# Kernel tuning notes

Hardware: AMD Instinct MI355X
Metric: run time of the kernel (lower is better)

Reference implementation:

```python
import jax, jax.numpy as jnp
import numpy as np

HEADS = 8

def _conv(x, w, b, stride, pad):
    # x: [B,C,H,W], w: [O,I,kh,kw] (torch OIHW layout)
    y = jax.lax.conv_general_dilated(x, w, (stride, stride), ((pad, pad), (pad, pad)),
                                     dimension_numbers=('NCHW', 'OIHW', 'NCHW'))
    return y + b[None, :, None, None]

def _maxpool2x2(x):
    # returns pooled values and one-hot argmax per 2x2 window (torch first-max tie-break)
    b, c, H, W = x.shape
    win = x.reshape(b, c, H // 2, 2, W // 2, 2).transpose(0, 1, 2, 4, 3, 5).reshape(b, c, H // 2, W // 2, 4)
    am = jnp.argmax(win, axis=-1)
    oh = jax.nn.one_hot(am, 4, dtype=x.dtype)
    pooled = jnp.sum(win * oh, axis=-1)
    return pooled, oh

def _maxunpool2x2(y, oh):
    b, c, h2, w2 = y.shape
    out = y[..., None] * oh  # [b,c,h2,w2,4]
    out = out.reshape(b, c, h2, w2, 2, 2).transpose(0, 1, 2, 4, 3, 5).reshape(b, c, h2 * 2, w2 * 2)
    return out

def _mha2d(x, wq, wk, wv, wo):
    # x: [b,c,h,w]; wq/wk/wv/wo stored as [in,out] so y = x @ W
    b, c, h, w = x.shape
    hw = h * w
    dk = wq.shape[1]
    dh = dk // HEADS
    xt = x.reshape(b, c, hw).transpose(0, 2, 1)  # [b,hw,c]
    def split(y):  # torch: view(b,hw,dh,heads).permute(0,3,1,2)
        return y.reshape(b, hw, dh, HEADS).transpose(0, 3, 1, 2)  # [b,heads,hw,dh]
    q = split(xt @ wq)
    k = split(xt @ wk)
    v = split(xt @ wv)
    scale = jnp.sqrt(jnp.asarray(dh, x.dtype))
    attn = jax.nn.softmax(jnp.einsum('bhqd,bhkd->bhqk', q, k) / scale, axis=-1)
    o = jnp.einsum('bhqk,bhkd->bhqd', attn, v)
    o = o.transpose(0, 2, 3, 1).reshape(b, hw, dk)  # [b,hw,dh,heads] -> merge
    o = o @ wo
    return o.transpose(0, 2, 1).reshape(b, dk, h, w)

def setup_inputs() -> dict:
    key = jax.random.key(0)
    ks = jax.random.split(key, 10)
    B, C, H, W = 16, 256, 64, 64
    s = 0.05
    return {
        'x': jax.random.normal(ks[0], (B, C, H, W), jnp.float32),
        'conv_w': jax.random.normal(ks[1], (C, C, 3, 3), jnp.float32) * s,
        'conv_b': jax.random.normal(ks[2], (C,), jnp.float32) * s,
        'fr_w': jax.random.normal(ks[3], (C, C, 1, 1), jnp.float32) * s,
        'fr_b': jax.random.normal(ks[4], (C,), jnp.float32) * s,
        'wq': jax.random.normal(ks[5], (C, C), jnp.float32) * s,
        'wk': jax.random.normal(ks[6], (C, C), jnp.float32) * s,
        'wv': jax.random.normal(ks[7], (C, C), jnp.float32) * s,
        'wo': jax.random.normal(ks[8], (C, C), jnp.float32) * s,
        'gamma': jax.random.normal(ks[9], (1,), jnp.float32) * 0.1,
    }

def reference(x, conv_w, conv_b, fr_w, fr_b, wq, wk, wv, wo, gamma):
    _x = _conv(x, fr_w, fr_b, 1, 0)          # 1x1 feature reduction
    _x, oh = _maxpool2x2(_x)                 # MaxPool2d(2, return_indices=True)
    _x = _mha2d(_x, wq, wk, wv, wo)          # attention over pooled grid
    _x = _maxunpool2x2(_x, oh)               # MaxUnpool2d(2)
    return _x * jnp.tanh(gamma[0]) + _conv(x, conv_w, conv_b, 1, 1)
```

## Files before the change

kernel.cpp:

```cpp
#include <hip/hip_runtime.h>
#include <hip/hip_bf16.h>
#include <math.h>

#define B 16
#define C 256
#define H 64
#define W 64
#define H2 32
#define W2 32
#define HW2 1024
#define HEADS 8
#define DH 32

typedef unsigned short ushort_t;
using short8 = __attribute__((ext_vector_type(8))) short;
using u16x8  = __attribute__((ext_vector_type(8))) unsigned short;
using f32x4  = __attribute__((ext_vector_type(4))) float;

__device__ inline ushort_t f2bf(float f) {
    __hip_bfloat16 hb = __float2bfloat16(f);
    return *(ushort_t*)&hb;
}
__device__ inline float bf2f(ushort_t u) {
    return __uint_as_float(((unsigned)u) << 16);
}

__device__ __forceinline__ void cp16(const ushort_t* g, ushort_t* l) {
    __builtin_amdgcn_global_load_lds(
        (const __attribute__((address_space(1))) void*)g,
        (__attribute__((address_space(3))) void*)l, 16, 0, 0);
}

#define RSCALE 0.17677669529663687f

__global__ __launch_bounds__(256) void k_prep_wT(const float* __restrict__ cw,
                                                 ushort_t* __restrict__ wbfT) {
    int i = threadIdx.x, o = blockIdx.x;
    const float* src = cw + ((size_t)o * C + i) * 9;
#pragma unroll
    for (int kk = 0; kk < 9; kk++)
        wbfT[((size_t)kk * C + o) * C + i] = f2bf(src[kk]);
}

__global__ __launch_bounds__(256) void k_prep_wx(
    const float* __restrict__ wq, const float* __restrict__ wk,
    const float* __restrict__ wv, const float* __restrict__ wo,
    const float* __restrict__ frw, ushort_t* __restrict__ wqkvT,
    ushort_t* __restrict__ woT, ushort_t* __restrict__ wfr) {
    int op = blockIdx.x, mat = blockIdx.y, t = threadIdx.x;
    if (mat < 3) {
        const float* w = (mat == 0) ? wq : (mat == 1) ? wk : wv;
        int hh = op >> 5, d = op & 31, col = d * 8 + hh;
        wqkvT[(size_t)mat * 65536 + op * 256 + t] = f2bf(w[t * 256 + col]);
    } else if (mat == 3) {
        int hh = t >> 5, d = t & 31, ic = d * 8 + hh;
        woT[op * 256 + t] = f2bf(wo[ic * 256 + op]);
    } else {
        wfr[op * 256 + t] = f2bf(frw[op * 256 + t]);
    }
}

__global__ __launch_bounds__(256) void k_prep_xn(const float* __restrict__ x,
                                                 ushort_t* __restrict__ xn) {
    __shared__ ushort_t ldsT[64 * 258];
    int t = threadIdx.x;
    int hp = blockIdx.x, b = blockIdx.y;
    ushort_t* dst = xn + ((size_t)(b * 66 + hp)) * 66 * 256;

    if (hp == 0 || hp == 65) {
        u16x8 z = (u16x8){0, 0, 0, 0, 0, 0, 0, 0};
        for (int i = t; i < 2112; i += 256) *(u16x8*)(dst + i * 8) = z;
        return;
    }
    const float* xb = x + ((size_t)b * 256) * 4096 + (size_t)(hp - 1) * 64;
    {
        int cq = t >> 6, w = t & 63;
#pragma unroll 8
        for (int it = 0; it < 64; ++it) {
            int c = it * 4 + cq;
            float v = xb[(size_t)c * 4096 + w];
            ldsT[w * 258 + c] = f2bf(v);
        }
    }
    __syncthreads();
    {
        u16x8 z = (u16x8){0, 0, 0, 0, 0, 0, 0, 0};
        if (t < 32) *(u16x8*)(dst + t * 8) = z;
        else if (t < 64) *(u16x8*)(dst + 65 * 256 + (t - 32) * 8) = z;
    }
    {
        int half = t >> 7, cl = t & 127;
#pragma unroll 4
        for (int it = 0; it < 32; ++it) {
            int w = it * 2 + half;
            unsigned v = *(const unsigned*)&ldsT[w * 258 + cl * 2];
            *(unsigned*)(dst + (size_t)(w + 1) * 256 + cl * 2) = v;
        }
    }
}

__global__ __launch_bounds__(256) void k_conv1pool_mfma(
    const ushort_t* __restrict__ xn, const ushort_t* __restrict__ wfr,
    const float* __restrict__ frb, ushort_t* __restrict__ Pbf,
    unsigned char* __restrict__ idx) {
    __shared__ __align__(16) ushort_t sh[32768];
    ushort_t* Als = sh;
    ushort_t* Bls = sh + 8192;
    int t = threadIdx.x;
    int wg = blockIdx.x;
    int mt = (wg & 7) * 64 + (wg >> 3);
    int b = mt >> 5;
    int h0 = (mt * 2) & 63;

    int r = t >> 2, p = t & 3;
    int kswz = (p ^ ((r >> 1) & 3)) * 8;
    const ushort_t* aB0 = xn + ((size_t)((b * 66 + h0 + 1) * 66 + (r + 1))) * 256 + kswz;
    const ushort_t* aB1 = xn + ((size_t)((b * 66 + h0 + 2) * 66 + (r + 1))) * 256 + kswz;
    const ushort_t* bB = wfr + (size_t)r * 256 + kswz;

    f32x4 acc[4][8];
#pragma unroll
    for (int mf = 0; mf < 4; mf++)
#pragma unroll
        for (int nf = 0; nf < 8; nf++) acc[mf][nf] = (f32x4){0.f, 0.f, 0.f, 0.f};

    cp16(aB0, &Als[t * 8]);
    cp16(aB1, &Als[2048 + t * 8]);
    cp16(bB, &Bls[t * 8]);
    cp16(bB + 64 * 256, &Bls[2048 + t * 8]);
    cp16(bB + 128 * 256, &Bls[4096 + t * 8]);
    cp16(bB + 192 * 256, &Bls[6144 + t * 8]);
    __syncthreads();

    int l = t & 63, wid = t >> 6, wm = wid >> 1, wn = wid & 1;
    int arow = wm * 64 + (l & 15);
    int brow = wn * 128 + (l & 15);
    int pslot = ((l >> 4) ^ ((l >> 1) & 3)) * 8;

    for (int s = 0; s < 8; s++) {
        int cur = s & 1;
        if (s < 7) {
            int off = (s + 1) * 32;
            int nb = cur ^ 1;
            cp16(aB0 + off, &Als[nb * 4096 + t * 8]);
            cp16(aB1 + off, &Als[nb * 4096 + 2048 + t * 8]);
            cp16(bB + off, &Bls[nb * 8192 + t * 8]);
            cp16(bB + 64 * 256 + off, &Bls[nb * 8192 + 2048 + t * 8]);
            cp16(bB + 128 * 256 + off, &Bls[nb * 8192 + 4096 + t * 8]);
            cp16(bB + 192 * 256 + off, &Bls[nb * 8192 + 6144 + t * 8]);
        }
        short8 af[4], bf[8];
#pragma unroll
        for (int mf = 0; mf < 4; mf++)
            af[mf] = *(const short8*)&Als[cur * 4096 + (arow + mf * 16) * 32 + pslot];
#pragma unroll
        for (int nf = 0; nf < 8; nf++)
            bf[nf] = *(const short8*)&Bls[cur * 8192 + (brow + nf * 16) * 32 + pslot];
#pragma unroll
        for (int mf = 0; mf < 4; mf++)
#pragma unroll
            for (int nf = 0; nf < 8; nf++)
                acc[mf][nf] = __builtin_amdgcn_mfma_f32_16x16x32_bf16(
                    af[mf], bf[nf], acc[mf][nf], 0, 0, 0);
        __syncthreads();
    }

#pragma unroll
    for (int nf = 0; nf < 8; nf++) {
        int o = wn * 128 + nf * 16 + (l & 15);
        float bias = frb[o];
#pragma unroll
        for (int mf = 0; mf < 4; mf++) {
            int rbase = wm * 64 + mf * 16 + ((l >> 4) << 2);
            f32x4 a = acc[mf][nf];
#pragma unroll
            for (int jj = 0; jj < 4; jj++)
                sh[(rbase + jj) * 256 + o] = f2bf(a[jj] + bias);
        }
    }
    __syncthreads();

    {
        int h2 = mt & 31;
        size_t rowb = (size_t)(b << 10) + h2 * 32;
        int o0 = (t & 31) * 8;
#pragma unroll
        for (int pp = 0; pp < 4; pp++) {
            int w2 = pp * 8 + (t >> 5);
            u16x8 r0 = *(const u16x8*)&sh[(2 * w2) * 256 + o0];
            u16x8 r1 = *(const u16x8*)&sh[(2 * w2 + 1) * 256 + o0];
            u16x8 r2 = *(const u16x8*)&sh[(64 + 2 * w2) * 256 + o0];
            u16x8 r3 = *(const u16x8*)&sh[(64 + 2 * w2 + 1) * 256 + o0];
            u16x8 pv;
            unsigned amlo = 0, amhi = 0;
#pragma unroll
            for (int e = 0; e < 8; e++) {
                float v0 = bf2f(r0[e]), v1 = bf2f(r1[e]);
                float v2 = bf2f(r2[e]), v3 = bf2f(r3[e]);
                float m = v0;
                ushort_t raw = r0[e];
                unsigned am = 0;
                if (v1 > m) { m = v1; raw = r1[e]; am = 1; }
                if (v2 > m) { m = v2; raw = r2[e]; am = 2; }
                if (v3 > m) { m = v3; raw = r3[e]; am = 3; }
                pv[e] = raw;
                if (e < 4) amlo |= am << (8 * e);
                else       amhi |= am << (8 * (e - 4));
            }
            size_t po = (rowb + w2) * 256 + o0;
            *(u16x8*)(Pbf + po) = pv;
            *(uint2*)(idx + po) = make_uint2(amlo, amhi);
        }
    }
}

__global__ __launch_bounds__(256) void k_qkv_mfma(
    const ushort_t* __restrict__ A, const ushort_t* __restrict__ Bw,
    ushort_t* __restrict__ qb, ushort_t* __restrict__ kb,
    ushort_t* __restrict__ vtb) {
    __shared__ __align__(16) ushort_t Als[2][4096];
    __shared__ __align__(16) ushort_t Bls[2][4096];
    int t = threadIdx.x;
    int wg = blockIdx.x;
    int linear = (wg & 7) * 96 + (wg >> 3);
    int mt = linear / 6, nt = linear % 6;

    int r = t >> 2, p = t & 3;
    int kswz = (p ^ ((r >> 1) & 3)) * 8;
    const ushort_t* aB0 = A + ((size_t)(mt * 128 + r)) * 256 + kswz;
    const ushort_t* aB1 = aB0 + (size_t)64 * 256;
    const ushort_t* bB0 = Bw + ((size_t)(nt * 128 + r)) * 256 + kswz;
    const ushort_t* bB1 = bB0 + (size_t)64 * 256;

    f32x4 acc[4][4];
#pragma unroll
    for (int mf = 0; mf < 4; mf++)
#pragma unroll
        for (int nf = 0; nf < 4; nf++) acc[mf][nf] = (f32x4){0.f, 0.f, 0.f, 0.f};

    cp16(aB0, &Als[0][t * 8]);
    cp16(aB1, &Als[0][2048 + t * 8]);
    cp16(bB0, &Bls[0][t * 8]);
    cp16(bB1, &Bls[0][2048 + t * 8]);
    __syncthreads();

    int l = t & 63, wid = t >> 6, wm = wid >> 1, wn = wid & 1;
    int arow = wm * 64 + (l & 15);
    int brow = wn * 64 + (l & 15);
    int pslot = ((l >> 4) ^ ((l >> 1) & 3)) * 8;

    for (int s = 0; s < 8; s++) {
        int cur = s & 1;
        if (s < 7) {
            int off = (s + 1) * 32;
            int nb = cur ^ 1;
            cp16(aB0 + off, &Als[nb][t * 8]);
            cp16(aB1 + off, &Als[nb][2048 + t * 8]);
            cp16(bB0 + off, &Bls[nb][t * 8]);
            cp16(bB1 + off, &Bls[nb][2048 + t * 8]);
        }
        short8 af[4], bf[4];
#pragma unroll
        for (int mf = 0; mf < 4; mf++)
            af[mf] = *(const short8*)&Als[cur][(arow + mf * 16) * 32 + pslot];
#pragma unroll
        for (int nf = 0; nf < 4; nf++)
            bf[nf] = *(const short8*)&Bls[cur][(brow + nf * 16) * 32 + pslot];
#pragma unroll
        for (int mf = 0; mf < 4; mf++)
#pragma unroll
            for (int nf = 0; nf < 4; nf++)
                acc[mf][nf] = __builtin_amdgcn_mfma_f32_16x16x32_bf16(
                    af[mf], bf[nf], acc[mf][nf], 0, 0, 0);
        __syncthreads();
    }

    if (nt < 4) {
        ushort_t* dst = (nt < 2) ? qb : kb;
        float sc = (nt < 2) ? RSCALE : 1.0f;
        int ccb = (nt & 1) * 128 + wn * 64;
#pragma unroll
        for (int nf = 0; nf < 4; nf++) {
            int cc = ccb + nf * 16 + (l & 15);
#pragma unroll
            for (int mf = 0; mf < 4; mf++) {
                int m = mt * 128 + wm * 64 + mf * 16 + ((l >> 4) << 2);
                f32x4 a = acc[mf][nf];
#pragma unroll
                for (int jj = 0; jj < 4; jj++)
                    dst[(size_t)(m + jj) * 256 + cc] = f2bf(a[jj] * sc);
            }
        }
    } else {
#pragma unroll
        for (int nf = 0; nf < 4; nf++) {
            int cc = (nt & 1) * 128 + wn * 64 + nf * 16 + (l & 15);
#pragma unroll
            for (int mf = 0; mf < 4; mf++) {
                int m = mt * 128 + wm * 64 + mf * 16 + ((l >> 4) << 2);
                int b = m >> 10, n0 = m & 1023;
                f32x4 a = acc[mf][nf];
                unsigned u0 = ((unsigned)f2bf(a[1]) << 16) | f2bf(a[0]);
                unsigned u1 = ((unsigned)f2bf(a[3]) << 16) | f2bf(a[2]);
                *(uint2*)&vtb[((size_t)(b * 256 + cc)) * 1024 + n0] =
                    make_uint2(u0, u1);
            }
        }
    }
}

__global__ __launch_bounds__(256) void k_attn_mfma(
    const ushort_t* __restrict__ qb, const ushort_t* __restrict__ kb,
    const ushort_t* __restrict__ vtb, ushort_t* __restrict__ aoT) {
    __shared__ __align__(16) ushort_t Klds[2][2048];
    __shared__ __align__(16) ushort_t Vlds[2][2048];
    __shared__ __align__(16) ushort_t Plds[4][2304];
    __shared__ float rs_lds[128];

    int t = threadIdx.x;
    int bid = blockIdx.x;
    int swz = (bid & 7) * 128 + (bid >> 3);
    int bh = swz >> 3, qt = swz & 7;
    int b = bh >> 3, h = bh & 7;
    int w = t >> 6, l = t & 63, g = l >> 4, li = l & 15;

    size_t qrow = (size_t)(b * 1024 + qt * 128 + w * 32 + li);
    short8 qv0 = *(const short8*)(qb + qrow * 256 + h * 32 + g * 8);
    short8 qv1 = *(const short8*)(qb + (qrow + 16) * 256 + h * 32 + g * 8);

    int sr = t >> 2, sp = t & 3;
    const ushort_t* kg =
        kb + ((size_t)(b * 1024 + sr)) * 256 + h * 32 + ((sp ^ ((sr >> 1) & 3)) * 8);
    int vd = t >> 3, vs = t & 7;
    const ushort_t* vg =
        vtb + ((size_t)(b * 256 + h * 32 + vd)) * 1024 + ((vs ^ (vd & 7)) * 8);

    f32x4 oacc[2][2];
    f32x4 rsv[2];
#pragma unroll
    for (int qf = 0; qf < 2; qf++) {
        rsv[qf] = (f32x4){0.f, 0.f, 0.f, 0.f};
#pragma unroll
        for (int df = 0; df < 2; df++) oacc[qf][df] = (f32x4){0.f, 0.f, 0.f, 0.f};
    }

    cp16(kg, &Klds[0][t * 8]);
    cp16(vg, &Vlds[0][t * 8]);
    __syncthreads();

    ushort_t* Pw = &Plds[w][0];

    for (int c = 0; c < 16; c++) {
        int cur = c & 1;
        if (c < 15) {
            cp16(kg + (size_t)(c + 1) * 64 * 256, &Klds[cur ^ 1][t * 8]);
            cp16(vg + (c + 1) * 64, &Vlds[cur ^ 1][t * 8]);
        }
        short8 ak[4];
#pragma unroll
        for (int kf = 0; kf < 4; kf++)
            ak[kf] = *(const short8*)&Klds[cur][(16 * kf + li) * 32 +
                                               ((g ^ ((l >> 1) & 3)) * 8)];
#pragma unroll
        for (int qf = 0; qf < 2; qf++) {
            short8 qv = qf ? qv1 : qv0;
#pragma unroll
            for (int kf = 0; kf < 4; kf++) {
                f32x4 st = __builtin_amdgcn_mfma_f32_16x16x32_bf16(
                    ak[kf], qv, (f32x4){0.f, 0.f, 0.f, 0.f}, 0, 0, 0);
                float p0 = __expf(st[0]), p1 = __expf(st[1]);
                float p2 = __expf(st[2]), p3 = __expf(st[3]);
                rsv[qf][0] += p0; rsv[qf][1] += p1;
                rsv[qf][2] += p2; rsv[qf][3] += p3;
                unsigned u0, u1;
                asm("v_cvt_pk_bf16_f32 %0, %1, %2" : "=v"(u0) : "v"(p0), "v"(p1));
                asm("v_cvt_pk_bf16_f32 %0, %1, %2" : "=v"(u1) : "v"(p2), "v"(p3));
                *(uint2*)&Pw[(16 * qf + li) * 72 + 16 * kf + 4 * g] =
                    make_uint2(u0, u1);
            }
        }
#pragma unroll
        for (int win = 0; win < 2; win++) {
            short8 pa[2], bv[2];
#pragma unroll
            for (int qf = 0; qf < 2; qf++)
                pa[qf] = *(const short8*)&Pw[(16 * qf + li) * 72 + win * 32 + 8 * g];
#pragma unroll
            for (int df = 0; df < 2; df++)
                bv[df] = *(const short8*)&Vlds[cur][(16 * df + li) * 64 +
                                                    (((win * 4 + g) ^ (l & 7)) * 8)];
#pragma unroll
            for (int qf = 0; qf < 2; qf++)
#pragma unroll
                for (int df = 0; df < 2; df++)
                    oacc[qf][df] = __builtin_amdgcn_mfma_f32_16x16x32_bf16(
                        pa[qf], bv[df], oacc[qf][df], 0, 0, 0);
        }
        __syncthreads();
    }

#pragma unroll
    for (int qf = 0; qf < 2; qf++) {
        float rs = (rsv[qf][0] + rsv[qf][1]) + (rsv[qf][2] + rsv[qf][3]);
        rs += __shfl_xor(rs, 16);
        rs += __shfl_xor(rs, 32);
        if (l < 16) rs_lds[w * 32 + 16 * qf + li] = rs;
    }
    __syncthreads();

#pragma unroll
    for (int qf = 0; qf < 2; qf++) {
        float4 rs4 = *(const float4*)&rs_lds[w * 32 + 16 * qf + 4 * g];
        float inv[4] = {1.f / rs4.x, 1.f / rs4.y, 1.f / rs4.z, 1.f / rs4.w};
#pragma unroll
        for (int df = 0; df < 2; df++) {
            f32x4 a = oacc[qf][df];
#pragma unroll
            for (int r2 = 0; r2 < 4; r2++) {
                size_t row = (size_t)(b * 1024 + qt * 128 + w * 32 + 16 * qf +
                                      4 * g + r2);
                aoT[row * 256 + h * 32 + 16 * df + li] = f2bf(a[r2] * inv[r2]);
            }
        }
    }
}

__global__ __launch_bounds__(256) void k_oproj_mfma(
    const ushort_t* __restrict__ A, const ushort_t* __restrict__ Bw,
    float* __restrict__ y2) {
    __shared__ __align__(16) ushort_t Als[2][4096];
    __shared__ __align__(16) ushort_t Bls[2][4096];
    int t = threadIdx.x;
    int wg = blockIdx.x;
    int linear = (wg & 7) * 32 + (wg >> 3);
    int nt = linear & 1, mt = linear >> 1;

    int r = t >> 2, p = t & 3;
    int kswz = (p ^ ((r >> 1) & 3)) * 8;
    const ushort_t* aB0 = A + ((size_t)(mt * 128 + r)) * 256 + kswz;
    const ushort_t* aB1 = aB0 + (size_t)64 * 256;
    const ushort_t* bB0 = Bw + ((size_t)(nt * 128 + r)) * 256 + kswz;
    const ushort_t* bB1 = bB0 + (size_t)64 * 256;

    f32x4 acc[4][4];
#pragma unroll
    for (int mf = 0; mf < 4; mf++)
#pragma unroll
        for (int nf = 0; nf < 4; nf++) acc[mf][nf] = (f32x4){0.f, 0.f, 0.f, 0.f};

    cp16(aB0, &Als[0][t * 8]);
    cp16(aB1, &Als[0][2048 + t * 8]);
    cp16(bB0, &Bls[0][t * 8]);
    cp16(bB1, &Bls[0][2048 + t * 8]);
    __syncthreads();

    int l = t & 63, wid = t >> 6, wm = wid >> 1, wn = wid & 1;
    int arow = wm * 64 + (l & 15);
    int brow = wn * 64 + (l & 15);
    int pslot = ((l >> 4) ^ ((l >> 1) & 3)) * 8;

    for (int s = 0; s < 8; s++) {
        int cur = s & 1;
        if (s < 7) {
            int off = (s + 1) * 32;
            int nb = cur ^ 1;
            cp16(aB0 + off, &Als[nb][t * 8]);
            cp16(aB1 + off, &Als[nb][2048 + t * 8]);
            cp16(bB0 + off, &Bls[nb][t * 8]);
            cp16(bB1 + off, &Bls[nb][2048 + t * 8]);
        }
        short8 af[4], bf[4];
#pragma unroll
        for (int mf = 0; mf < 4; mf++)
            af[mf] = *(const short8*)&Als[cur][(arow + mf * 16) * 32 + pslot];
#pragma unroll
        for (int nf = 0; nf < 4; nf++)
            bf[nf] = *(const short8*)&Bls[cur][(brow + nf * 16) * 32 + pslot];
#pragma unroll
        for (int mf = 0; mf < 4; mf++)
#pragma unroll
            for (int nf = 0; nf < 4; nf++)
                acc[mf][nf] = __builtin_amdgcn_mfma_f32_16x16x32_bf16(
                    af[mf], bf[nf], acc[mf][nf], 0, 0, 0);
        __syncthreads();
    }

#pragma unroll
    for (int nf = 0; nf < 4; nf++) {
        int cc = nt * 128 + wn * 64 + nf * 16 + (l & 15);
#pragma unroll
        for (int mf = 0; mf < 4; mf++) {
            int m = mt * 128 + wm * 64 + mf * 16 + ((l >> 4) << 2);
            f32x4 a = acc[mf][nf];
#pragma unroll
            for (int jj = 0; jj < 4; jj++)
                y2[(size_t)(m + jj) * 256 + cc] = a[jj];
        }
    }
}

__global__ __launch_bounds__(512) void k_conv3_mfma(
    const ushort_t* __restrict__ xn, const ushort_t* __restrict__ wbfT,
    const float* __restrict__ cb, const float* __restrict__ y2,
    const unsigned char* __restrict__ idx, const float* __restrict__ gamma,
    float* __restrict__ out) {
    extern __shared__ __align__(16) ushort_t lds[];
    ushort_t* AL = lds;
    ushort_t* BL = lds + 32768;
    int t = threadIdx.x;
    int mt = blockIdx.x;

    int srow = t >> 3, sslot = t & 7;
    int kel = (sslot ^ (srow & 7)) * 8;
    const ushort_t* aP[2][2];
    const ushort_t* bP[2][2];
#pragma unroll
    for (int hf = 0; hf < 2; hf++)
#pragma unroll
        for (int j = 0; j < 2; j++) {
            int row = hf * 128 + j * 64 + srow;
            int m = mt * 256 + row;
            int b0 = m >> 12, h0 = (m >> 6) & 63, w0 = m & 63;
            aP[hf][j] = xn + ((size_t)((b0 * 66 + h0) * 66 + w0)) * 256 + kel;
            bP[hf][j] = wbfT + (size_t)row * 256 + kel;
        }

    auto offA = [](int kt) -> int {
        int it = kt / 9, khkw = kt - it * 9;
        int kh = khkw / 3, kw = khkw - kh * 3;
        return (kh * 66 + kw) * 256 + it * 64;
    };
    auto offB = [](int kt) -> int {
        int it = kt / 9, khkw = kt - it * 9;
        return khkw * 65536 + it * 64;
    };
    auto STAGE_A = [&](int bb, int hf, int kt) {
        int o = offA(kt);
        ushort_t* d = AL + bb * 16384 + hf * 8192 + t * 8;
        cp16(aP[hf][0] + o, d);
        cp16(aP[hf][1] + o, d + 4096);
    };
    auto STAGE_B = [&](int bb, int hf, int kt) {
        int o = offB(kt);
        ushort_t* d = BL + bb * 16384 + hf * 8192 + t * 8;
        cp16(bP[hf][0] + o, d);
        cp16(bP[hf][1] + o, d + 4096);
    };

    f32x4 acc[8][4];
#pragma unroll
    for (int mf = 0; mf < 8; mf++)
#pragma unroll
        for (int nf = 0; nf < 4; nf++) acc[mf][nf] = (f32x4){0.f, 0.f, 0.f, 0.f};

    int l = t & 63, wid = t >> 6, wm = wid >> 2, wn = wid & 3;
    int lr = l & 15, g = l >> 4, l7 = l & 7;
    int abase = wm * 8192;
    int bbase = (wn >> 1) * 8192 + (wn & 1) * 4096;

    short8 aLo[4][2], aHi[4][2], bf0[2][2], bf1[2][2];

    auto RD_A = [&](short8 (&fa)[4][2], const ushort_t* Ab, int ah) {
#pragma unroll
        for (int mf = 0; mf < 4; mf++)
#pragma unroll
            for (int kk = 0; kk < 2; kk++)
                fa[mf][kk] = *(const short8*)
                    &Ab[(ah * 64 + mf * 16 + lr) * 64 + (((kk * 4 + g) ^ l7) * 8)];
    };
    auto RD_B = [&](short8 (&fb)[2][2], const ushort_t* Bb, int bh) {
#pragma unroll
        for (int nf = 0; nf < 2; nf++)
#pragma unroll
            for (int kk = 0; kk < 2; kk++)
                fb[nf][kk] = *(const short8*)
                    &Bb[(bh * 32 + nf * 16 + lr) * 64 + (((kk * 4 + g) ^ l7) * 8)];
    };
    auto MFMAH = [&](short8 (&fa)[4][2], int mo) {
        __builtin_amdgcn_s_setprio(1);
#pragma unroll
        for (int kk = 0; kk < 2; kk++)
#pragma unroll
            for (int mf = 0; mf < 4; mf++)
#pragma unroll
                for (int nf = 0; nf < 2; nf++)
                    acc[mf + mo][nf] = __builtin_amdgcn_mfma_f32_16x16x32_bf16(
                        fa[mf][kk], bf0[nf][kk], acc[mf + mo][nf], 0, 0, 0);
#pragma unroll
        for (int kk = 0; kk < 2; kk++)
#pragma unroll
            for (int mf = 0; mf < 4; mf++)
#pragma unroll
                for (int nf = 0; nf < 2; nf++)
                    acc[mf + mo][nf + 2] = __builtin_amdgcn_mfma_f32_16x16x32_bf16(
                        fa[mf][kk], bf1[nf][kk], acc[mf + mo][nf + 2], 0, 0, 0);
        __builtin_amdgcn_s_setprio(0);
    };
    auto BARW = [&]() {
        __builtin_amdgcn_sched_barrier(0);
        __builtin_amdgcn_s_barrier();
        __builtin_amdgcn_sched_barrier(0);
    };

    STAGE_A(0, 0, 0); STAGE_A(0, 1, 0); STAGE_B(0, 0, 0); STAGE_B(0, 1, 0);
    STAGE_A(1, 0, 1); STAGE_A(1, 1, 1);
    asm volatile("s_waitcnt vmcnt(4)" ::: "memory");
    __builtin_amdgcn_s_barrier();
    RD_A(aLo, AL + abase, 0);
    RD_B(bf0, BL + bbase, 0);
    RD_B(bf1, BL + bbase, 1);

    for (int kt = 0; kt < 36; kt++) {
        int cur = kt & 1, nxt = cur ^ 1;
        const ushort_t* Ac = AL + cur * 16384 + abase;
        const ushort_t* An = AL + nxt * 16384 + abase;
        const ushort_t* Bn = BL + nxt * 16384 + bbase;
        BARW();
        if (kt < 35) { STAGE_B(nxt, 0, kt + 1); STAGE_B(nxt, 1, kt + 1); }
        RD_A(aHi, Ac, 1);
        MFMAH(aLo, 0);
        asm volatile("s_waitcnt vmcnt(0)" ::: "memory");
        BARW();
        if (kt < 34) { STAGE_A(cur, 0, kt + 2); STAGE_A(cur, 1, kt + 2); }
        if (kt < 35) RD_A(aLo, An, 0);
        MFMAH(aHi, 4);
        if (kt < 35) { RD_B(bf0, Bn, 0); RD_B(bf1, Bn, 1); }
    }

    float tg = tanhf(gamma[0]);
    int mbase = mt * 256 + wm * 128 + (g << 2);
    int obase = wn * 64 + lr;
#pragma unroll
    for (int nf = 0; nf < 4; nf++) {
        int o = obase + nf * 16;
        float bias = cb[o];
#pragma unroll
        for (int mf = 0; mf < 8; mf++) {
            int m = mbase + mf * 16;
            int b = m >> 12, h = (m >> 6) & 63, w0 = m & 63;
            const unsigned char* idr = idx + ((size_t)(b << 10)) * 256;
            const float* y2r = y2 + ((size_t)(b << 10)) * 256;
            f32x4 a = acc[mf][nf];
            float v4[4];
#pragma unroll
            for (int jj = 0; jj < 4; jj++) {
                int wj = w0 + jj;
                int n2 = ((h >> 1) << 5) + (wj >> 1);
                int j2 = ((h & 1) << 1) + (wj & 1);
                float val = a[jj] + bias;
                if (idr[(size_t)n2 * 256 + o] == (unsigned char)j2)
                    val += tg * y2r[(size_t)n2 * 256 + o];
                v4[jj] = val;
            }
            *(float4*)(out + (((size_t)(b * C + o) * H + h) << 6) + w0) =
                make_float4(v4[0], v4[1], v4[2], v4[3]);
        }
    }
}

extern "C" void kernel_launch(void* const* d_in, const int* in_sizes, int n_in,
                              void* d_out, int out_size, void* d_ws, size_t ws_size,
                              hipStream_t stream) {
    const float* x      = (const float*)d_in[0];
    const float* conv_w = (const float*)d_in[1];
    const float* conv_b = (const float*)d_in[2];
    const float* fr_w   = (const float*)d_in[3];
    const float* fr_b   = (const float*)d_in[4];
    const float* wq     = (const float*)d_in[5];
    const float* wk     = (const float*)d_in[6];
    const float* wv     = (const float*)d_in[7];
    const float* wo     = (const float*)d_in[8];
    const float* gamma  = (const float*)d_in[9];
    float* out = (float*)d_out;
    char* ws = (char*)d_ws;

    ushort_t* wbfT  = (ushort_t*)(ws + 0);
    ushort_t* wfrbf = (ushort_t*)(ws + 1179648);
    ushort_t* wqkvT = (ushort_t*)(ws + 1310720);
    ushort_t* woT   = (ushort_t*)(ws + 1703936);
    ushort_t* xn    = (ushort_t*)(ws + 2097152);
    ushort_t* Pbf   = (ushort_t*)(ws + 37781504);
    unsigned char* idx = (unsigned char*)(ws + 46170112);
    ushort_t* qb    = (ushort_t*)(ws + 50364416);
    ushort_t* kb    = (ushort_t*)(ws + 58753024);
    ushort_t* vtb   = (ushort_t*)(ws + 67141632);
    ushort_t* aoT   = (ushort_t*)(ws + 75530240);
    float* y2       = (float*)(ws + 50364416);

    k_prep_wT<<<dim3(C), dim3(256), 0, stream>>>(conv_w, wbfT);
    k_prep_wx<<<dim3(256, 5), dim3(256), 0, stream>>>(wq, wk, wv, wo, fr_w,
                                                      wqkvT, woT, wfrbf);
    k_prep_xn<<<dim3(66, B), dim3(256), 0, stream>>>(x, xn);
    k_conv1pool_mfma<<<dim3(512), dim3(256), 0, stream>>>(xn, wfrbf, fr_b, Pbf, idx);
    k_qkv_mfma<<<dim3(768), dim3(256), 0, stream>>>(Pbf, wqkvT, qb, kb, vtb);
    k_attn_mfma<<<dim3(1024), dim3(256), 0, stream>>>(qb, kb, vtb, aoT);
    k_oproj_mfma<<<dim3(256), dim3(256), 0, stream>>>(aoT, woT, y2);
    (void)hipFuncSetAttribute(reinterpret_cast<const void*>(k_conv3_mfma),
                              hipFuncAttributeMaxDynamicSharedMemorySize, 131072);
    k_conv3_mfma<<<dim3(256), dim3(512), 131072, stream>>>(xn, wbfT, conv_b, y2, idx,
                                                           gamma, out);
    (void)in_sizes; (void)n_in; (void)out_size; (void)ws_size;
}
```

Measured before the change: 218.0 us.

## Stage a halo window of the input once per channel chunk in conv3

The 3x3 conv kernel used to re-load a shifted 256-row input tile from global memory for every kernel tap. It now stages a 6x66 halo window of padded input for each 64-channel chunk into LDS. All nine taps read that shared window at shifted offsets, and only the weight tiles stay double-buffered per tap. This is meant to cut global/L2 traffic for the activation operand roughly ninefold. The cost is a non-overlapped window load with extra barriers at each channel-chunk boundary.

```diff
diff --git a/kernel.cpp b/kernel.cpp
--- a/kernel.cpp
+++ b/kernel.cpp
@@ -505,46 +505,40 @@
     const unsigned char* __restrict__ idx, const float* __restrict__ gamma,
     float* __restrict__ out) {
     extern __shared__ __align__(16) ushort_t lds[];
-    ushort_t* AL = lds;
-    ushort_t* BL = lds + 32768;
+    ushort_t* WL = lds;
+    ushort_t* BL = lds + 28672;
     int t = threadIdx.x;
     int mt = blockIdx.x;
+    int bb0 = mt >> 4;
+    int h0w = (mt * 4) & 63;
 
     int srow = t >> 3, sslot = t & 7;
-    int kel = (sslot ^ (srow & 7)) * 8;
-    const ushort_t* aP[2][2];
+    int kelB = (sslot ^ (srow & 7)) * 8;
     const ushort_t* bP[2][2];
 #pragma unroll
     for (int hf = 0; hf < 2; hf++)
 #pragma unroll
-        for (int j = 0; j < 2; j++) {
-            int row = hf * 128 + j * 64 + srow;
-            int m = mt * 256 + row;
-            int b0 = m >> 12, h0 = (m >> 6) & 63, w0 = m & 63;
-            aP[hf][j] = xn + ((size_t)((b0 * 66 + h0) * 66 + w0)) * 256 + kel;
-            bP[hf][j] = wbfT + (size_t)row * 256 + kel;
-        }
-
-    auto offA = [](int kt) -> int {
-        int it = kt / 9, khkw = kt - it * 9;
-        int kh = khkw / 3, kw = khkw - kh * 3;
-        return (kh * 66 + kw) * 256 + it * 64;
+        for (int j = 0; j < 2; j++)
+            bP[hf][j] = wbfT + (size_t)(hf * 128 + j * 64 + srow) * 256 + kelB;
+
+    auto STAGE_B = [&](int bb, int off) {
+        ushort_t* d = BL + bb * 16384 + t * 8;
+        cp16(bP[0][0] + off, d);
+        cp16(bP[0][1] + off, d + 4096);
+        cp16(bP[1][0] + off, d + 8192);
+        cp16(bP[1][1] + off, d + 12288);
     };
-    auto offB = [](int kt) -> int {
-        int it = kt / 9, khkw = kt - it * 9;
-        return khkw * 65536 + it * 64;
-    };
-    auto STAGE_A = [&](int bb, int hf, int kt) {
-        int o = offA(kt);
-        ushort_t* d = AL + bb * 16384 + hf * 8192 + t * 8;
-        cp16(aP[hf][0] + o, d);
-        cp16(aP[hf][1] + o, d + 4096);
-    };
-    auto STAGE_B = [&](int bb, int hf, int kt) {
-        int o = offB(kt);
-        ushort_t* d = BL + bb * 16384 + hf * 8192 + t * 8;
-        cp16(bP[hf][0] + o, d);
-        cp16(bP[hf][1] + o, d + 4096);
+
+    auto STAGE_W = [&](int it) {
+#pragma unroll
+        for (int p = 0; p < 7; ++p) {
+            int r = p * 64 + (t >> 3);
+            int hh = r / 66, ww = r - hh * 66;
+            const ushort_t* g = xn +
+                ((size_t)((bb0 * 66 + h0w + hh) * 66 + ww)) * 256 + it * 64 +
+                ((sslot ^ (ww & 7)) * 8);
+            cp16(g, WL + p * 4096 + t * 8);
+        }
     };
 
     f32x4 acc[8][4];
@@ -555,18 +549,20 @@
 
     int l = t & 63, wid = t >> 6, wm = wid >> 2, wn = wid & 3;
     int lr = l & 15, g = l >> 4, l7 = l & 7;
-    int abase = wm * 8192;
     int bbase = (wn >> 1) * 8192 + (wn & 1) * 4096;
 
     short8 aLo[4][2], aHi[4][2], bf0[2][2], bf1[2][2];
 
-    auto RD_A = [&](short8 (&fa)[4][2], const ushort_t* Ab, int ah) {
+    auto RD_AW = [&](short8 (&fa)[4][2], int kh, int kw, int hf2) {
+        int hl = wm * 2 + hf2 + kh;
 #pragma unroll
         for (int mf = 0; mf < 4; mf++)
 #pragma unroll
-            for (int kk = 0; kk < 2; kk++)
+            for (int kk = 0; kk < 2; kk++) {
+                int c = mf * 16 + lr + kw;
                 fa[mf][kk] = *(const short8*)
-                    &Ab[(ah * 64 + mf * 16 + lr) * 64 + (((kk * 4 + g) ^ l7) * 8)];
+                    &WL[hl * 4224 + c * 64 + (((kk * 4 + g) ^ (c & 7)) * 8)];
+            }
     };
     auto RD_B = [&](short8 (&fb)[2][2], const ushort_t* Bb, int bh) {
 #pragma unroll
@@ -602,29 +598,49 @@
         __builtin_amdgcn_sched_barrier(0);
     };
 
-    STAGE_A(0, 0, 0); STAGE_A(0, 1, 0); STAGE_B(0, 0, 0); STAGE_B(0, 1, 0);
-    STAGE_A(1, 0, 1); STAGE_A(1, 1, 1);
-    asm volatile("s_waitcnt vmcnt(4)" ::: "memory");
-    __builtin_amdgcn_s_barrier();
-    RD_A(aLo, AL + abase, 0);
+    STAGE_W(0);
+    STAGE_B(0, 0);
+    asm volatile("s_waitcnt vmcnt(0)" ::: "memory");
+    BARW();
+    RD_AW(aLo, 0, 0, 0);
     RD_B(bf0, BL + bbase, 0);
     RD_B(bf1, BL + bbase, 1);
 
-    for (int kt = 0; kt < 36; kt++) {
-        int cur = kt & 1, nxt = cur ^ 1;
-        const ushort_t* Ac = AL + cur * 16384 + abase;
-        const ushort_t* An = AL + nxt * 16384 + abase;
-        const ushort_t* Bn = BL + nxt * 16384 + bbase;
-        BARW();
-        if (kt < 35) { STAGE_B(nxt, 0, kt + 1); STAGE_B(nxt, 1, kt + 1); }
-        RD_A(aHi, Ac, 1);
-        MFMAH(aLo, 0);
-        asm volatile("s_waitcnt vmcnt(0)" ::: "memory");
-        BARW();
-        if (kt < 34) { STAGE_A(cur, 0, kt + 2); STAGE_A(cur, 1, kt + 2); }
-        if (kt < 35) RD_A(aLo, An, 0);
-        MFMAH(aHi, 4);
-        if (kt < 35) { RD_B(bf0, Bn, 0); RD_B(bf1, Bn, 1); }
+    int bufp = 0;
+    for (int it = 0; it < 4; ++it) {
+#pragma unroll
+        for (int khkw = 0; khkw < 9; ++khkw) {
+            const int kh = khkw / 3, kw = khkw - kh * 3;
+            int kt = it * 9 + khkw;
+            int nxtb = bufp ^ 1;
+            if (kt < 35) {
+                int noff = ((khkw == 8) ? 0 : (khkw + 1)) * 65536 +
+                           ((khkw == 8) ? (it + 1) : it) * 64;
+                STAGE_B(nxtb, noff);
+            }
+            RD_AW(aHi, kh, kw, 1);
+            MFMAH(aLo, 0);
+            __builtin_amdgcn_sched_barrier(0);
+            asm volatile("s_waitcnt vmcnt(0)" ::: "memory");
+            BARW();
+            if (khkw < 8) {
+                const int nkh = (khkw + 1) / 3, nkw = (khkw + 1) - nkh * 3;
+                RD_AW(aLo, nkh, nkw, 0);
+            }
+            MFMAH(aHi, 4);
+            if (kt < 35) {
+                RD_B(bf0, BL + nxtb * 16384 + bbase, 0);
+                RD_B(bf1, BL + nxtb * 16384 + bbase, 1);
+            }
+            bufp = nxtb;
+        }
+        if (it < 3) {
+            BARW();
+            STAGE_W(it + 1);
+            asm volatile("s_waitcnt vmcnt(0)" ::: "memory");
+            BARW();
+            RD_AW(aLo, 0, 0, 0);
+        }
     }
 
     float tg = tanhf(gamma[0]);
@@ -697,7 +713,7 @@
     k_oproj_mfma<<<dim3(256), dim3(256), 0, stream>>>(aoT, woT, y2);
     (void)hipFuncSetAttribute(reinterpret_cast<const void*>(k_conv3_mfma),
                               hipFuncAttributeMaxDynamicSharedMemorySize, 131072);
-    k_conv3_mfma<<<dim3(256), dim3(512), 131072, stream>>>(xn, wbfT, conv_b, y2, idx,
+    k_conv3_mfma<<<dim3(256), dim3(512), 122880, stream>>>(xn, wbfT, conv_b, y2, idx,
                                                            gamma, out);
     (void)in_sizes; (void)n_in; (void)out_size; (void)ws_size;
 }
```

Measured after the change: 250.2 us. +14.8%, slower.
